# Optimization experiments

Measured on AMD Instinct MI355X. Metric: run time of the kernel, lower is better.

The kernel has to match this reference:

```python
import jax, jax.numpy as jnp
import numpy as np

H = 8  # num heads (init_kwargs)

def setup_inputs() -> dict:
    key = jax.random.key(0)
    ks = jax.random.split(key, 12)
    B, L, D = 2, 256, 512
    dk = D // H
    s = 0.02
    return {
        "query": jax.random.normal(ks[0], (B, L, D), jnp.float32),
        "key": jax.random.normal(ks[1], (B, L, D), jnp.float32),
        "value": jax.random.normal(ks[2], (B, L, D), jnp.float32),
        "mask": jnp.ones((B, L, L), jnp.int32),
        "relative_q": jax.random.normal(ks[3], (B * H, L, L, dk), jnp.float32) * s,
        "relative_v": jax.random.normal(ks[4], (B * H, L, L, dk), jnp.float32) * s,
        "Wq": jax.random.normal(ks[5], (D, D), jnp.float32) * s,
        "bq": jnp.zeros((D,), jnp.float32),
        "Wk": jax.random.normal(ks[6], (D, D), jnp.float32) * s,
        "bk": jnp.zeros((D,), jnp.float32),
        "Wv": jax.random.normal(ks[7], (D, D), jnp.float32) * s,
        "bv": jnp.zeros((D,), jnp.float32),
        "Wo": jax.random.normal(ks[8], (D, D), jnp.float32) * s,
        "bo": jnp.zeros((D,), jnp.float32),
    }


def reference(query, key, value, mask, relative_q, relative_v,
              Wq, bq, Wk, bk, Wv, bv, Wo, bo):
    B, L, D = query.shape
    dk = D // H
    scale = 1.0 / jnp.sqrt(jnp.asarray(dk, query.dtype))

    def proj(x, W, b):
        # torch Linear: x @ W^T + b, then split heads -> [B*H, L, dk]
        y = jnp.einsum('bld,ed->ble', x, W) + b
        return y.reshape(B, L, H, dk).transpose(0, 2, 1, 3).reshape(B * H, L, dk)

    q = proj(query, Wq, bq)
    k = proj(key, Wk, bk)
    v = proj(value, Wv, bv)

    # scores [B*H, L, L]
    scores = jnp.einsum('bid,bjd->bij', q, k) * scale
    # relative_q bias: q_i . rel_q[i, j] per (batch*head)
    scores = scores + jnp.einsum('bid,bijd->bij', q, relative_q)

    mask_bh = jnp.repeat(mask[:, None], H, axis=1).reshape(B * H, L, L)
    neg = jnp.asarray(-1e9, scores.dtype)
    scores = jnp.where(mask_bh == 0, neg, scores)

    p = jax.nn.softmax(scores, axis=-1)  # dropout is identity at eval

    ctx = jnp.einsum('bij,bjd->bid', p, v)
    ctx = ctx + jnp.einsum('bij,bijd->bid', p, relative_v)

    ctx = ctx.reshape(B, H, L, dk).transpose(0, 2, 1, 3).reshape(B, L, D)
    return jnp.einsum('bld,ed->ble', ctx, Wo) + bo
```

## Files before the change

kernel.cpp:

```cpp
#include <hip/hip_runtime.h>

#define L_SEQ 256
#define D_MODEL 512
#define N_HEADS 8
#define DK 64
#define N_BATCH 2
#define BH (N_BATCH * N_HEADS)

__global__ __launch_bounds__(256) void proj_gemm(
    const float* __restrict__ X0, const float* __restrict__ X1, const float* __restrict__ X2,
    const float* __restrict__ W0, const float* __restrict__ W1, const float* __restrict__ W2,
    const float* __restrict__ B0, const float* __restrict__ B1, const float* __restrict__ B2,
    float* __restrict__ O0, float* __restrict__ O1, float* __restrict__ O2,
    int split_heads)
{
    const int z = blockIdx.z;
    const float* X    = (z == 0) ? X0 : (z == 1) ? X1 : X2;
    const float* W    = (z == 0) ? W0 : (z == 1) ? W1 : W2;
    const float* bias = (z == 0) ? B0 : (z == 1) ? B1 : B2;
    float* out        = (z == 0) ? O0 : (z == 1) ? O1 : O2;

    __shared__ float Xs[32][36];
    __shared__ float Ws[32][36];

    const int t = threadIdx.x;
    const int row0 = blockIdx.x * 32;
    const int col0 = blockIdx.y * 32;
    const int lr = t >> 3;
    const int lc = (t & 7) << 2;
    const int r0 = (t >> 4) * 2;
    const int c0 = (t & 15) * 2;

    float a00 = 0.f, a01 = 0.f, a10 = 0.f, a11 = 0.f;

    for (int k0 = 0; k0 < 512; k0 += 32) {
        __syncthreads();
        *(float4*)&Xs[lr][lc] = *(const float4*)&X[(size_t)(row0 + lr) * 512 + k0 + lc];
        *(float4*)&Ws[lr][lc] = *(const float4*)&W[(size_t)(col0 + lr) * 512 + k0 + lc];
        __syncthreads();
#pragma unroll
        for (int kk = 0; kk < 32; kk += 4) {
            const float4 x0 = *(const float4*)&Xs[r0][kk];
            const float4 x1 = *(const float4*)&Xs[r0 + 1][kk];
            const float4 w0 = *(const float4*)&Ws[c0][kk];
            const float4 w1 = *(const float4*)&Ws[c0 + 1][kk];
            a00 = fmaf(x0.x, w0.x, fmaf(x0.y, w0.y, fmaf(x0.z, w0.z, fmaf(x0.w, w0.w, a00))));
            a01 = fmaf(x0.x, w1.x, fmaf(x0.y, w1.y, fmaf(x0.z, w1.z, fmaf(x0.w, w1.w, a01))));
            a10 = fmaf(x1.x, w0.x, fmaf(x1.y, w0.y, fmaf(x1.z, w0.z, fmaf(x1.w, w0.w, a10))));
            a11 = fmaf(x1.x, w1.x, fmaf(x1.y, w1.y, fmaf(x1.z, w1.z, fmaf(x1.w, w1.w, a11))));
        }
    }

    const float accs[2][2] = {{a00, a01}, {a10, a11}};
#pragma unroll
    for (int dr = 0; dr < 2; ++dr) {
#pragma unroll
        for (int dc = 0; dc < 2; ++dc) {
            const int row = row0 + r0 + dr;
            const int c   = col0 + c0 + dc;
            const float val = accs[dr][dc] + bias[c];
            if (split_heads) {
                const int b = row >> 8, l = row & 255;
                const int h = c >> 6,  d = c & 63;
                out[(size_t)((b * N_HEADS + h) * L_SEQ + l) * DK + d] = val;
            } else {
                out[(size_t)row * 512 + c] = val;
            }
        }
    }
}

__global__ __launch_bounds__(256) void attn_fused(
    const float* __restrict__ q, const float* __restrict__ k,
    const float* __restrict__ v, const int* __restrict__ mask,
    const float* __restrict__ relq, const float* __restrict__ relv,
    float* __restrict__ ctx)
{
    const int bh = blockIdx.x >> 8;
    const int i  = blockIdx.x & 255;
    const int b  = bh >> 3;
    const int h  = bh & 7;

    const int t    = threadIdx.x;
    const int lane = t & 63;
    const int wave = t >> 6;

    __shared__ float q_s[64];
    __shared__ float sc[256];
    __shared__ float red[8];
    __shared__ float ctxp[4][64];

    if (t < 64) q_s[t] = q[(size_t)(bh * L_SEQ + i) * DK + t];
    __syncthreads();

    const int jgrp = t >> 4;
    const int d0   = (t & 15) << 2;

    const float q0 = q_s[d0], q1 = q_s[d0 + 1], q2 = q_s[d0 + 2], q3 = q_s[d0 + 3];

    const float* relq_row = relq + ((size_t)bh * L_SEQ + i) * L_SEQ * DK;
    const float* k_base   = k + (size_t)bh * L_SEQ * DK;
    const int* mask_row   = mask + (size_t)(b * L_SEQ + i) * L_SEQ;
    const float scale = 0.125f;

#pragma unroll 4
    for (int p = 0; p < 16; ++p) {
        const int j = p * 16 + jgrp;
        const float4 rq = *(const float4*)&relq_row[(size_t)j * DK + d0];
        const float4 kv = *(const float4*)&k_base[(size_t)j * DK + d0];
        const float t0 = fmaf(scale, kv.x, rq.x);
        const float t1 = fmaf(scale, kv.y, rq.y);
        const float t2 = fmaf(scale, kv.z, rq.z);
        const float t3 = fmaf(scale, kv.w, rq.w);
        float s = fmaf(q0, t0, fmaf(q1, t1, fmaf(q2, t2, q3 * t3)));
        s += __shfl_xor(s, 1);
        s += __shfl_xor(s, 2);
        s += __shfl_xor(s, 4);
        s += __shfl_xor(s, 8);
        if ((t & 15) == 0) {
            const int m = mask_row[j];
            sc[j] = (m == 0) ? -1e9f : s;
        }
    }
    __syncthreads();

    const float s_own = sc[t];
    float mval = s_own;
#pragma unroll
    for (int o = 32; o >= 1; o >>= 1) mval = fmaxf(mval, __shfl_xor(mval, o));
    if (lane == 0) red[wave] = mval;
    __syncthreads();
    mval = fmaxf(fmaxf(red[0], red[1]), fmaxf(red[2], red[3]));

    const float e = __expf(s_own - mval);
    float ssum = e;
#pragma unroll
    for (int o = 32; o >= 1; o >>= 1) ssum += __shfl_xor(ssum, o);
    if (lane == 0) red[4 + wave] = ssum;
    __syncthreads();
    ssum = red[4] + red[5] + red[6] + red[7];

    sc[t] = e / ssum;
    __syncthreads();

    const float* relv_row = relv + ((size_t)bh * L_SEQ + i) * L_SEQ * DK;
    const float* v_base   = v + (size_t)bh * L_SEQ * DK;

    float a0 = 0.f, a1 = 0.f, a2 = 0.f, a3 = 0.f;
#pragma unroll 4
    for (int p = 0; p < 16; ++p) {
        const int j = p * 16 + jgrp;
        const float4 rv = *(const float4*)&relv_row[(size_t)j * DK + d0];
        const float4 vv = *(const float4*)&v_base[(size_t)j * DK + d0];
        const float pw = sc[j];
        a0 = fmaf(pw, rv.x + vv.x, a0);
        a1 = fmaf(pw, rv.y + vv.y, a1);
        a2 = fmaf(pw, rv.z + vv.z, a2);
        a3 = fmaf(pw, rv.w + vv.w, a3);
    }
    a0 += __shfl_xor(a0, 16); a0 += __shfl_xor(a0, 32);
    a1 += __shfl_xor(a1, 16); a1 += __shfl_xor(a1, 32);
    a2 += __shfl_xor(a2, 16); a2 += __shfl_xor(a2, 32);
    a3 += __shfl_xor(a3, 16); a3 += __shfl_xor(a3, 32);
    if (lane < 16) {
        ctxp[wave][lane * 4 + 0] = a0;
        ctxp[wave][lane * 4 + 1] = a1;
        ctxp[wave][lane * 4 + 2] = a2;
        ctxp[wave][lane * 4 + 3] = a3;
    }
    __syncthreads();

    if (t < 64) {
        const float r = ctxp[0][t] + ctxp[1][t] + ctxp[2][t] + ctxp[3][t];
        ctx[(size_t)(b * L_SEQ + i) * D_MODEL + h * DK + t] = r;
    }
}

extern "C" void kernel_launch(void* const* d_in, const int* in_sizes, int n_in,
                              void* d_out, int out_size, void* d_ws, size_t ws_size,
                              hipStream_t stream) {
    const float* query = (const float*)d_in[0];
    const float* key   = (const float*)d_in[1];
    const float* value = (const float*)d_in[2];
    const int*   mask  = (const int*)d_in[3];
    const float* relq  = (const float*)d_in[4];
    const float* relv  = (const float*)d_in[5];
    const float* Wq = (const float*)d_in[6];
    const float* bq = (const float*)d_in[7];
    const float* Wk = (const float*)d_in[8];
    const float* bk = (const float*)d_in[9];
    const float* Wv = (const float*)d_in[10];
    const float* bv = (const float*)d_in[11];
    const float* Wo = (const float*)d_in[12];
    const float* bo = (const float*)d_in[13];
    float* out = (float*)d_out;

    float* ws = (float*)d_ws;
    const size_t QKV = (size_t)BH * L_SEQ * DK;
    float* q_ws   = ws;
    float* k_ws   = ws + QKV;
    float* v_ws   = ws + 2 * QKV;
    float* ctx_ws = ws + 3 * QKV;

    proj_gemm<<<dim3(16, 16, 3), 256, 0, stream>>>(
        query, key, value, Wq, Wk, Wv, bq, bk, bv, q_ws, k_ws, v_ws, 1);

    attn_fused<<<BH * L_SEQ, 256, 0, stream>>>(q_ws, k_ws, v_ws, mask,
                                               relq, relv, ctx_ws);

    proj_gemm<<<dim3(16, 16, 1), 256, 0, stream>>>(
        ctx_ws, ctx_ws, ctx_ws, Wo, Wo, Wo, bo, bo, bo, out, out, out, 0);
}
```

Measured before the change: 585.6 us.

## Process four query rows per attention block and prefetch GEMM tiles in registers

The attention kernel now handles four query rows per block, so each K and V row is loaded once and reused across four rows, while relq and relv are streamed for every row. Softmax reductions are batched across the four rows, and mask loads move into the softmax phase. The projection GEMM widens its K tile to 64 and prefetches the next tile into registers while computing the current one. The main cost, streaming the large relq and relv tensors, is unchanged, so gains depend mostly on fewer blocks, less K/V traffic and more memory-level parallelism, at the price of higher register pressure.

```diff
diff --git a/kernel.cpp b/kernel.cpp
--- a/kernel.cpp
+++ b/kernel.cpp
@@ -6,6 +6,7 @@
 #define DK 64
 #define N_BATCH 2
 #define BH (N_BATCH * N_HEADS)
+#define ROWS 4
 
 __global__ __launch_bounds__(256) void proj_gemm(
     const float* __restrict__ X0, const float* __restrict__ X1, const float* __restrict__ X2,
@@ -20,26 +21,42 @@
     const float* bias = (z == 0) ? B0 : (z == 1) ? B1 : B2;
     float* out        = (z == 0) ? O0 : (z == 1) ? O1 : O2;
 
-    __shared__ float Xs[32][36];
-    __shared__ float Ws[32][36];
+    __shared__ float Xs[32][72];
+    __shared__ float Ws[32][72];
 
     const int t = threadIdx.x;
     const int row0 = blockIdx.x * 32;
     const int col0 = blockIdx.y * 32;
     const int lr = t >> 3;
-    const int lc = (t & 7) << 2;
+    const int lc = (t & 7) << 3;
     const int r0 = (t >> 4) * 2;
     const int c0 = (t & 15) * 2;
 
+    const float* Xrow = X + (size_t)(row0 + lr) * 512 + lc;
+    const float* Wrow = W + (size_t)(col0 + lr) * 512 + lc;
+
+    float4 cX0 = *(const float4*)&Xrow[0];
+    float4 cX1 = *(const float4*)&Xrow[4];
+    float4 cW0 = *(const float4*)&Wrow[0];
+    float4 cW1 = *(const float4*)&Wrow[4];
+
     float a00 = 0.f, a01 = 0.f, a10 = 0.f, a11 = 0.f;
 
-    for (int k0 = 0; k0 < 512; k0 += 32) {
+    for (int k0 = 0; k0 < 512; k0 += 64) {
         __syncthreads();
-        *(float4*)&Xs[lr][lc] = *(const float4*)&X[(size_t)(row0 + lr) * 512 + k0 + lc];
-        *(float4*)&Ws[lr][lc] = *(const float4*)&W[(size_t)(col0 + lr) * 512 + k0 + lc];
+        *(float4*)&Xs[lr][lc]     = cX0;
+        *(float4*)&Xs[lr][lc + 4] = cX1;
+        *(float4*)&Ws[lr][lc]     = cW0;
+        *(float4*)&Ws[lr][lc + 4] = cW1;
         __syncthreads();
-#pragma unroll
-        for (int kk = 0; kk < 32; kk += 4) {
+        if (k0 + 64 < 512) {
+            cX0 = *(const float4*)&Xrow[k0 + 64];
+            cX1 = *(const float4*)&Xrow[k0 + 68];
+            cW0 = *(const float4*)&Wrow[k0 + 64];
+            cW1 = *(const float4*)&Wrow[k0 + 68];
+        }
+#pragma unroll
+        for (int kk = 0; kk < 64; kk += 4) {
             const float4 x0 = *(const float4*)&Xs[r0][kk];
             const float4 x1 = *(const float4*)&Xs[r0 + 1][kk];
             const float4 w0 = *(const float4*)&Ws[c0][kk];
@@ -76,8 +93,8 @@
     const float* __restrict__ relq, const float* __restrict__ relv,
     float* __restrict__ ctx)
 {
-    const int bh = blockIdx.x >> 8;
-    const int i  = blockIdx.x & 255;
+    const int bh = blockIdx.x >> 6;
+    const int i0 = (blockIdx.x & 63) * ROWS;
     const int b  = bh >> 3;
     const int h  = bh & 7;
 
@@ -85,94 +102,139 @@
     const int lane = t & 63;
     const int wave = t >> 6;
 
-    __shared__ float q_s[64];
-    __shared__ float sc[256];
-    __shared__ float red[8];
-    __shared__ float ctxp[4][64];
-
-    if (t < 64) q_s[t] = q[(size_t)(bh * L_SEQ + i) * DK + t];
+    __shared__ float q_s[ROWS][64];
+    __shared__ float sc[ROWS][256];
+    __shared__ float red[2][ROWS][4];
+    __shared__ float ctxp[ROWS][4][64];
+
+    {
+        const int r = t >> 6, d = t & 63;
+        q_s[r][d] = q[((size_t)bh * L_SEQ + i0 + r) * DK + d];
+    }
     __syncthreads();
 
     const int jgrp = t >> 4;
     const int d0   = (t & 15) << 2;
 
-    const float q0 = q_s[d0], q1 = q_s[d0 + 1], q2 = q_s[d0 + 2], q3 = q_s[d0 + 3];
-
-    const float* relq_row = relq + ((size_t)bh * L_SEQ + i) * L_SEQ * DK;
-    const float* k_base   = k + (size_t)bh * L_SEQ * DK;
-    const int* mask_row   = mask + (size_t)(b * L_SEQ + i) * L_SEQ;
+    float4 qr[ROWS];
+#pragma unroll
+    for (int r = 0; r < ROWS; ++r) qr[r] = *(const float4*)&q_s[r][d0];
+
+    const float* kb = k + (size_t)bh * L_SEQ * DK;
+    const float* vb = v + (size_t)bh * L_SEQ * DK;
+    const size_t relbase = ((size_t)bh * L_SEQ + i0) * L_SEQ * DK;
     const float scale = 0.125f;
 
-#pragma unroll 4
+#pragma unroll 2
     for (int p = 0; p < 16; ++p) {
         const int j = p * 16 + jgrp;
-        const float4 rq = *(const float4*)&relq_row[(size_t)j * DK + d0];
-        const float4 kv = *(const float4*)&k_base[(size_t)j * DK + d0];
-        const float t0 = fmaf(scale, kv.x, rq.x);
-        const float t1 = fmaf(scale, kv.y, rq.y);
-        const float t2 = fmaf(scale, kv.z, rq.z);
-        const float t3 = fmaf(scale, kv.w, rq.w);
-        float s = fmaf(q0, t0, fmaf(q1, t1, fmaf(q2, t2, q3 * t3)));
-        s += __shfl_xor(s, 1);
-        s += __shfl_xor(s, 2);
-        s += __shfl_xor(s, 4);
-        s += __shfl_xor(s, 8);
-        if ((t & 15) == 0) {
-            const int m = mask_row[j];
-            sc[j] = (m == 0) ? -1e9f : s;
-        }
-    }
-    __syncthreads();
-
-    const float s_own = sc[t];
-    float mval = s_own;
-#pragma unroll
-    for (int o = 32; o >= 1; o >>= 1) mval = fmaxf(mval, __shfl_xor(mval, o));
-    if (lane == 0) red[wave] = mval;
-    __syncthreads();
-    mval = fmaxf(fmaxf(red[0], red[1]), fmaxf(red[2], red[3]));
-
-    const float e = __expf(s_own - mval);
-    float ssum = e;
-#pragma unroll
-    for (int o = 32; o >= 1; o >>= 1) ssum += __shfl_xor(ssum, o);
-    if (lane == 0) red[4 + wave] = ssum;
-    __syncthreads();
-    ssum = red[4] + red[5] + red[6] + red[7];
-
-    sc[t] = e / ssum;
-    __syncthreads();
-
-    const float* relv_row = relv + ((size_t)bh * L_SEQ + i) * L_SEQ * DK;
-    const float* v_base   = v + (size_t)bh * L_SEQ * DK;
-
-    float a0 = 0.f, a1 = 0.f, a2 = 0.f, a3 = 0.f;
-#pragma unroll 4
+        const float4 kv = *(const float4*)&kb[(size_t)j * DK + d0];
+        float4 rq[ROWS];
+#pragma unroll
+        for (int r = 0; r < ROWS; ++r)
+            rq[r] = *(const float4*)&relq[relbase + ((size_t)r * L_SEQ + j) * DK + d0];
+#pragma unroll
+        for (int r = 0; r < ROWS; ++r) {
+            const float t0 = fmaf(scale, kv.x, rq[r].x);
+            const float t1 = fmaf(scale, kv.y, rq[r].y);
+            const float t2 = fmaf(scale, kv.z, rq[r].z);
+            const float t3 = fmaf(scale, kv.w, rq[r].w);
+            float s = fmaf(qr[r].x, t0, fmaf(qr[r].y, t1, fmaf(qr[r].z, t2, qr[r].w * t3)));
+            s += __shfl_xor(s, 1);
+            s += __shfl_xor(s, 2);
+            s += __shfl_xor(s, 4);
+            s += __shfl_xor(s, 8);
+            if ((t & 15) == 0) sc[r][j] = s;
+        }
+    }
+    __syncthreads();
+
+    const int* mb = mask + (size_t)b * L_SEQ * L_SEQ + (size_t)i0 * L_SEQ;
+    float sraw[ROWS], e[ROWS];
+#pragma unroll
+    for (int r = 0; r < ROWS; ++r) {
+        const int mk = mb[(size_t)r * L_SEQ + t];
+        sraw[r] = (mk == 0) ? -1e9f : sc[r][t];
+    }
+    {
+        float mv[ROWS];
+#pragma unroll
+        for (int r = 0; r < ROWS; ++r) mv[r] = sraw[r];
+#pragma unroll
+        for (int o = 32; o >= 1; o >>= 1)
+#pragma unroll
+            for (int r = 0; r < ROWS; ++r) mv[r] = fmaxf(mv[r], __shfl_xor(mv[r], o));
+        if (lane == 0)
+#pragma unroll
+            for (int r = 0; r < ROWS; ++r) red[0][r][wave] = mv[r];
+    }
+    __syncthreads();
+#pragma unroll
+    for (int r = 0; r < ROWS; ++r) {
+        const float M = fmaxf(fmaxf(red[0][r][0], red[0][r][1]),
+                              fmaxf(red[0][r][2], red[0][r][3]));
+        e[r] = __expf(sraw[r] - M);
+    }
+    {
+        float sm[ROWS];
+#pragma unroll
+        for (int r = 0; r < ROWS; ++r) sm[r] = e[r];
+#pragma unroll
+        for (int o = 32; o >= 1; o >>= 1)
+#pragma unroll
+            for (int r = 0; r < ROWS; ++r) sm[r] += __shfl_xor(sm[r], o);
+        if (lane == 0)
+#pragma unroll
+            for (int r = 0; r < ROWS; ++r) red[1][r][wave] = sm[r];
+    }
+    __syncthreads();
+#pragma unroll
+    for (int r = 0; r < ROWS; ++r) {
+        const float S = red[1][r][0] + red[1][r][1] + red[1][r][2] + red[1][r][3];
+        sc[r][t] = e[r] / S;
+    }
+    __syncthreads();
+
+    float4 acc[ROWS];
+#pragma unroll
+    for (int r = 0; r < ROWS; ++r) acc[r] = make_float4(0.f, 0.f, 0.f, 0.f);
+
+#pragma unroll 2
     for (int p = 0; p < 16; ++p) {
         const int j = p * 16 + jgrp;
-        const float4 rv = *(const float4*)&relv_row[(size_t)j * DK + d0];
-        const float4 vv = *(const float4*)&v_base[(size_t)j * DK + d0];
-        const float pw = sc[j];
-        a0 = fmaf(pw, rv.x + vv.x, a0);
-        a1 = fmaf(pw, rv.y + vv.y, a1);
-        a2 = fmaf(pw, rv.z + vv.z, a2);
-        a3 = fmaf(pw, rv.w + vv.w, a3);
-    }
-    a0 += __shfl_xor(a0, 16); a0 += __shfl_xor(a0, 32);
-    a1 += __shfl_xor(a1, 16); a1 += __shfl_xor(a1, 32);
-    a2 += __shfl_xor(a2, 16); a2 += __shfl_xor(a2, 32);
-    a3 += __shfl_xor(a3, 16); a3 += __shfl_xor(a3, 32);
-    if (lane < 16) {
-        ctxp[wave][lane * 4 + 0] = a0;
-        ctxp[wave][lane * 4 + 1] = a1;
-        ctxp[wave][lane * 4 + 2] = a2;
-        ctxp[wave][lane * 4 + 3] = a3;
-    }
-    __syncthreads();
-
-    if (t < 64) {
-        const float r = ctxp[0][t] + ctxp[1][t] + ctxp[2][t] + ctxp[3][t];
-        ctx[(size_t)(b * L_SEQ + i) * D_MODEL + h * DK + t] = r;
+        const float4 vv = *(const float4*)&vb[(size_t)j * DK + d0];
+        float4 rv[ROWS];
+#pragma unroll
+        for (int r = 0; r < ROWS; ++r)
+            rv[r] = *(const float4*)&relv[relbase + ((size_t)r * L_SEQ + j) * DK + d0];
+#pragma unroll
+        for (int r = 0; r < ROWS; ++r) {
+            const float pw = sc[r][j];
+            acc[r].x = fmaf(pw, vv.x + rv[r].x, acc[r].x);
+            acc[r].y = fmaf(pw, vv.y + rv[r].y, acc[r].y);
+            acc[r].z = fmaf(pw, vv.z + rv[r].z, acc[r].z);
+            acc[r].w = fmaf(pw, vv.w + rv[r].w, acc[r].w);
+        }
+    }
+#pragma unroll
+    for (int r = 0; r < ROWS; ++r) {
+        acc[r].x += __shfl_xor(acc[r].x, 16); acc[r].x += __shfl_xor(acc[r].x, 32);
+        acc[r].y += __shfl_xor(acc[r].y, 16); acc[r].y += __shfl_xor(acc[r].y, 32);
+        acc[r].z += __shfl_xor(acc[r].z, 16); acc[r].z += __shfl_xor(acc[r].z, 32);
+        acc[r].w += __shfl_xor(acc[r].w, 16); acc[r].w += __shfl_xor(acc[r].w, 32);
+        if (lane < 16) {
+            ctxp[r][wave][lane * 4 + 0] = acc[r].x;
+            ctxp[r][wave][lane * 4 + 1] = acc[r].y;
+            ctxp[r][wave][lane * 4 + 2] = acc[r].z;
+            ctxp[r][wave][lane * 4 + 3] = acc[r].w;
+        }
+    }
+    __syncthreads();
+
+    {
+        const int r = t >> 6, d = t & 63;
+        const float o = ctxp[r][0][d] + ctxp[r][1][d] + ctxp[r][2][d] + ctxp[r][3][d];
+        ctx[((size_t)b * L_SEQ + i0 + r) * D_MODEL + h * DK + d] = o;
     }
 }
 
@@ -205,8 +267,8 @@
     proj_gemm<<<dim3(16, 16, 3), 256, 0, stream>>>(
         query, key, value, Wq, Wk, Wv, bq, bk, bv, q_ws, k_ws, v_ws, 1);
 
-    attn_fused<<<BH * L_SEQ, 256, 0, stream>>>(q_ws, k_ws, v_ws, mask,
-                                               relq, relv, ctx_ws);
+    attn_fused<<<BH * (L_SEQ / ROWS), 256, 0, stream>>>(q_ws, k_ws, v_ws, mask,
+                                                        relq, relv, ctx_ws);
 
     proj_gemm<<<dim3(16, 16, 1), 256, 0, stream>>>(
         ctx_ws, ctx_ws, ctx_ws, Wo, Wo, Wo, bo, bo, bo, out, out, out, 0);
```

Result: faster. 566.1 us (-3.3%).
